# Kernel tuning notes

Hardware: AMD Instinct MI355X
Metric: run time of the kernel (lower is better)

## Reference

```python
import jax, jax.numpy as jnp
import numpy as np
import math

DIM = 2048
N_HEADS = 16
HEAD_DIM = DIM // N_HEADS
BASE = 10000
B, S = 2, 2048


def rope_cache(seq_len, head_dim, base):
    theta = 1.0 / (base ** (jnp.arange(0, head_dim, 2, dtype=jnp.float32)[: head_dim // 2] / head_dim))
    idx_theta = jnp.arange(seq_len, dtype=jnp.float32)[:, None] * theta[None, :]  # [S, D/2]
    return jnp.cos(idx_theta), jnp.sin(idx_theta)


def apply_rope(x, cos, sin):
    # x: [B, S, H, D]; cos/sin: [S, D/2]; interleaved-pair rotation
    b, s, h, d = x.shape
    xr = x.astype(jnp.float32).reshape(b, s, h, d // 2, 2)
    c = cos[None, :, None, :]
    sn = sin[None, :, None, :]
    x0, x1 = xr[..., 0], xr[..., 1]
    out = jnp.stack([x0 * c - x1 * sn, x1 * c + x0 * sn], axis=-1)
    return out.reshape(b, s, h, d).astype(x.dtype)


def setup_inputs() -> dict:
    key = jax.random.key(0)
    k1, k2, k3, k4, k5 = jax.random.split(key, 5)
    x = jax.random.normal(k1, (B, S, DIM), dtype=jnp.float32)
    # causal mask: True = masked out (strict upper triangle)
    mask = jnp.triu(jnp.ones((S, S), dtype=bool), k=1)[None, None]  # [1,1,S,S]
    scale = 0.02
    wq = jax.random.normal(k2, (DIM, DIM), dtype=jnp.float32) * scale
    wk = jax.random.normal(k3, (DIM, DIM), dtype=jnp.float32) * scale
    wv = jax.random.normal(k4, (DIM, DIM), dtype=jnp.float32) * scale
    wo = jax.random.normal(k5, (DIM, DIM), dtype=jnp.float32) * scale
    return {"x": x, "mask": mask, "wq": wq, "wk": wk, "wv": wv, "wo": wo}


def reference(x, mask, wq, wk, wv, wo):
    b, s, _ = x.shape
    cos, sin = rope_cache(s, HEAD_DIM, BASE)
    q = (x @ wq.T).reshape(b, s, N_HEADS, HEAD_DIM)
    k = (x @ wk.T).reshape(b, s, N_HEADS, HEAD_DIM)
    v = (x @ wv.T).reshape(b, s, N_HEADS, HEAD_DIM)
    q = apply_rope(q, cos, sin)
    k = apply_rope(k, cos, sin)
    # [B, H, S, S]
    scores = jnp.einsum('bqhd,bkhd->bhqk', q, k) / math.sqrt(HEAD_DIM)
    scores = jnp.where(mask, -jnp.inf, scores)
    attn = jax.nn.softmax(scores.astype(jnp.float32), axis=-1).astype(q.dtype)
    out = jnp.einsum('bhqk,bkhd->bqhd', attn, v).reshape(b, s, DIM)
    return out @ wo.T
```

## Files before the change

### kernel.cpp

```cpp
#include <hip/hip_runtime.h>
#include <hip/hip_bf16.h>
#include <math.h>

#define DIM   2048
#define NH    16
#define HD    128
#define SEQ   2048
#define BATCH 2
#define QKVN  6144

typedef __attribute__((ext_vector_type(8))) short short8;
typedef __attribute__((ext_vector_type(4))) float f32x4;
typedef __attribute__((ext_vector_type(4))) unsigned int u32x4;
typedef __attribute__((ext_vector_type(4))) _Float16 half4;

static __device__ __forceinline__ unsigned short f2bf(float f) {
    __hip_bfloat16 h = __float2bfloat16(f);
    return *reinterpret_cast<unsigned short*>(&h);
}

static __device__ __forceinline__ void gload16(const void* g, void* l) {
    __builtin_amdgcn_global_load_lds(
        (const __attribute__((address_space(1))) void*)(g),
        (__attribute__((address_space(3))) void*)(l), 16, 0, 0);
}

__device__ __forceinline__ void storeC_helper(float* C, size_t idx, float v) { C[idx] = v; }
__device__ __forceinline__ void storeC_helper(__hip_bfloat16* C, size_t idx, float v) { C[idx] = __float2bfloat16(v); }

__global__ __launch_bounds__(256) void cast_all(const float* __restrict__ x,
                                                const float* __restrict__ wq,
                                                const float* __restrict__ wk,
                                                const float* __restrict__ wv,
                                                const float* __restrict__ wo,
                                                __hip_bfloat16* __restrict__ xb,
                                                __hip_bfloat16* __restrict__ wqkvb,
                                                __hip_bfloat16* __restrict__ wob) {
    const int VX = (BATCH * SEQ * DIM) / 4;
    const int VW = (DIM * DIM) / 4;
    int v = blockIdx.x * blockDim.x + threadIdx.x;
    const float* src; __hip_bfloat16* dst; int off;
    if (v < VX)               { src = x;  dst = xb;                            off = v; }
    else if (v < VX + VW)     { src = wq; dst = wqkvb;                         off = v - VX; }
    else if (v < VX + 2 * VW) { src = wk; dst = wqkvb + (size_t)DIM * DIM;     off = v - VX - VW; }
    else if (v < VX + 3 * VW) { src = wv; dst = wqkvb + 2ull * DIM * DIM;      off = v - VX - 2 * VW; }
    else                      { src = wo; dst = wob;                           off = v - VX - 3 * VW; }
    float4 f = *(const float4*)(src + (size_t)off * 4);
    union { unsigned short u[4]; uint2 d; } pk;
    pk.u[0] = f2bf(f.x); pk.u[1] = f2bf(f.y); pk.u[2] = f2bf(f.z); pk.u[3] = f2bf(f.w);
    *(uint2*)(dst + (size_t)off * 4) = pk.d;
}

template <int MODE, typename OutT>
__global__ __launch_bounds__(256) void gemm_bt(const __hip_bfloat16* __restrict__ A,
                                               const __hip_bfloat16* __restrict__ B,
                                               OutT* __restrict__ C,
                                               _Float16* __restrict__ vt,
                                               int M, int N, int K) {
    constexpr int BK = 64;
    __shared__ __align__(16) __hip_bfloat16 As[128 * BK];
    __shared__ __align__(16) __hip_bfloat16 Bs[128 * BK];
    int tid  = threadIdx.x;
    int lane = tid & 63;
    int wave = tid >> 6;
    int quad = lane >> 4;
    int l15  = lane & 15;
    int wr   = wave >> 1, wc = wave & 1;
    int m0 = blockIdx.y * 128;
    int n0 = blockIdx.x * 128;
    f32x4 acc[4][4] = {};

    for (int k0 = 0; k0 < K; k0 += BK) {
        __syncthreads();
#pragma unroll
        for (int c = 0; c < 4; c++) {
            int br = (wave * 4 + c) * 8;
            int r  = br + (lane >> 3);
            int cc = (lane & 7) ^ (r & 7);
            gload16(A + (size_t)(m0 + r) * K + k0 + cc * 8, As + br * 64);
            gload16(B + (size_t)(n0 + r) * K + k0 + cc * 8, Bs + br * 64);
        }
        __syncthreads();
#pragma unroll
        for (int kk = 0; kk < BK; kk += 32) {
            short8 af[4], bf4[4];
#pragma unroll
            for (int t = 0; t < 4; t++) {
                int Ra = wr * 64 + t * 16 + l15;
                int pa = ((kk >> 3) + quad) ^ (Ra & 7);
                af[t] = *(const short8*)(As + Ra * 64 + pa * 8);
                int Rb = wc * 64 + t * 16 + l15;
                int pb = ((kk >> 3) + quad) ^ (Rb & 7);
                bf4[t] = *(const short8*)(Bs + Rb * 64 + pb * 8);
            }
#pragma unroll
            for (int mt = 0; mt < 4; mt++)
#pragma unroll
                for (int nt = 0; nt < 4; nt++)
                    acc[mt][nt] = __builtin_amdgcn_mfma_f32_16x16x32_bf16(af[mt], bf4[nt], acc[mt][nt], 0, 0, 0);
        }
    }

    if (MODE == 1 && n0 >= 4096) {
        __syncthreads();
        _Float16* T = ((wave < 2) ? (_Float16*)As : (_Float16*)Bs) + (wave & 1) * 4096;
#pragma unroll
        for (int mt = 0; mt < 4; mt++)
#pragma unroll
            for (int nt = 0; nt < 4; nt++) {
                int dcol = nt * 16 + l15;
#pragma unroll
                for (int r = 0; r < 4; r++) {
                    int row = mt * 16 + quad * 4 + r;
                    int chunk = (row >> 3) ^ (dcol & 7);
                    T[dcol * 64 + chunk * 8 + (row & 7)] = (_Float16)acc[mt][nt][r];
                }
            }
        int h = (n0 - 4096) >> 7;
        int b = m0 >> 11;
        int sbase = (m0 & (SEQ - 1)) + wr * 64;
#pragma unroll
        for (int pass = 0; pass < 8; pass++) {
            int dl = pass * 8 + (lane >> 3);
            int sc = lane & 7;
            int chunk = sc ^ (dl & 7);
            u32x4 val = *(const u32x4*)(T + dl * 64 + chunk * 8);
            int d = wc * 64 + dl;
            *(u32x4*)(vt + ((size_t)((b * NH + h) * HD + d)) * SEQ + sbase + sc * 8) = val;
        }
        return;
    }

#pragma unroll
    for (int nt = 0; nt < 4; nt++) {
        int col = n0 + wc * 64 + nt * 16 + l15;
        float theta = 0.f;
        if (MODE == 1)
            theta = __expf(-((float)((col & 127) & ~1) * (1.0f / (float)HD)) * 9.210340371976184f);
#pragma unroll
        for (int mt = 0; mt < 4; mt++)
#pragma unroll
            for (int r = 0; r < 4; r++) {
                int row = m0 + wr * 64 + mt * 16 + quad * 4 + r;
                float val = acc[mt][nt][r];
                if (MODE == 1) {
                    float part = __shfl_xor(val, 1);
                    int s = row & (SEQ - 1);
                    float sn, cs;
                    __sincosf((float)s * theta, &sn, &cs);
                    val = (l15 & 1) ? val * cs + part * sn : val * cs - part * sn;
                }
                storeC_helper(C, (size_t)row * N + col, val);
            }
    }
}

__global__ __launch_bounds__(256, 2) void flash_kernel(const __hip_bfloat16* __restrict__ qkv,
                                                       const _Float16* __restrict__ vt,
                                                       __hip_bfloat16* __restrict__ attn) {
    __shared__ __align__(16) __hip_bfloat16 Ks[2][64 * 128];
    __shared__ __align__(16) _Float16 Vts[2][128 * 64];
    int tid  = threadIdx.x;
    int lane = tid & 63;
    int wl   = tid >> 6;
    int quad = lane >> 4;
    int l15  = lane & 15;
    int qt = 15 - blockIdx.x;
    int bh = blockIdx.y;
    int b  = bh >> 4;
    int h  = bh & 15;
    size_t row0 = (size_t)b * SEQ;
    const _Float16* vbase = vt + (size_t)bh * HD * SEQ;
    const float scale = 0.08838834764831845f;
    const float NEG = -1e30f;

    auto stage = [&](int buf, int kt) {
#pragma unroll
        for (int c = 0; c < 4; c++) {
            int br = (wl * 4 + c) * 4;
            int r  = br + (lane >> 4);
            int cc = (lane & 15) ^ (r & 15);
            gload16(qkv + (row0 + kt * 64 + r) * (size_t)QKVN + DIM + h * HD + cc * 8,
                    &Ks[buf][br * 128]);
        }
#pragma unroll
        for (int c = 0; c < 4; c++) {
            int br = (wl * 4 + c) * 8;
            int r  = br + (lane >> 3);
            int cc = (lane & 7) ^ ((r >> 1) & 7);
            gload16(vbase + (size_t)r * SEQ + kt * 64 + cc * 8, &Vts[buf][br * 64]);
        }
    };

    int ntiles = 2 * (qt + 1);

    short8 qf[2][4];
#pragma unroll
    for (int mt = 0; mt < 2; mt++) {
        int qrow = qt * 128 + wl * 32 + mt * 16 + l15;
        const __hip_bfloat16* qptr = qkv + (row0 + qrow) * (size_t)QKVN + h * HD + quad * 8;
#pragma unroll
        for (int c = 0; c < 4; c++) qf[mt][c] = *(const short8*)(qptr + c * 32);
    }
    f32x4 o[2][8] = {};
    float m_[2] = {NEG, NEG}, l_[2] = {0.f, 0.f};

    stage(0, 0);

    for (int i = 0; i < ntiles; i++) {
        __syncthreads();
        if (i + 1 < ntiles) stage((i + 1) & 1, i + 1);
        const __hip_bfloat16* ks = Ks[i & 1];
        const _Float16* vts = Vts[i & 1];

        f32x4 s[2][4] = {};
#pragma unroll
        for (int ktile = 0; ktile < 4; ktile++) {
            int R = ktile * 16 + l15;
#pragma unroll
            for (int c = 0; c < 4; c++) {
                int phys = (c * 4 + quad) ^ (R & 15);
                short8 kf = *(const short8*)(ks + R * 128 + phys * 8);
                s[0][ktile] = __builtin_amdgcn_mfma_f32_16x16x32_bf16(kf, qf[0][c], s[0][ktile], 0, 0, 0);
                s[1][ktile] = __builtin_amdgcn_mfma_f32_16x16x32_bf16(kf, qf[1][c], s[1][ktile], 0, 0, 0);
            }
        }
        bool diag = (i >= 2 * qt);
        float alpha[2];
#pragma unroll
        for (int mt = 0; mt < 2; mt++) {
            int q = qt * 128 + wl * 32 + mt * 16 + l15;
#pragma unroll
            for (int ktile = 0; ktile < 4; ktile++)
#pragma unroll
                for (int r = 0; r < 4; r++) {
                    float v = s[mt][ktile][r] * scale;
                    if (diag) {
                        int key = i * 64 + ktile * 16 + quad * 4 + r;
                        if (key > q) v = NEG;
                    }
                    s[mt][ktile][r] = v;
                }
            float v = s[mt][0][0];
#pragma unroll
            for (int ktile = 0; ktile < 4; ktile++)
#pragma unroll
                for (int r = 0; r < 4; r++) v = fmaxf(v, s[mt][ktile][r]);
            v = fmaxf(v, __shfl_xor(v, 16));
            v = fmaxf(v, __shfl_xor(v, 32));
            float mnew = fmaxf(m_[mt], v);
            alpha[mt] = __expf(m_[mt] - mnew);
            m_[mt] = mnew;
            float sum = 0.f;
#pragma unroll
            for (int ktile = 0; ktile < 4; ktile++)
#pragma unroll
                for (int r = 0; r < 4; r++) {
                    float p = __expf(s[mt][ktile][r] - mnew);
                    s[mt][ktile][r] = p;
                    sum += p;
                }
            sum += __shfl_xor(sum, 16);
            sum += __shfl_xor(sum, 32);
            l_[mt] = l_[mt] * alpha[mt] + sum;
#pragma unroll
            for (int dt = 0; dt < 8; dt++) o[mt][dt] *= alpha[mt];
        }
        half4 pk[2][4];
#pragma unroll
        for (int mt = 0; mt < 2; mt++)
#pragma unroll
            for (int kc = 0; kc < 4; kc++)
#pragma unroll
                for (int r = 0; r < 4; r++) pk[mt][kc][r] = (_Float16)s[mt][kc][r];
#pragma unroll
        for (int kc = 0; kc < 4; kc++)
#pragma unroll
            for (int dt = 0; dt < 8; dt++) {
                int d = dt * 16 + l15;
                int c4 = ((kc * 4 + quad) ^ (d & 14));
                half4 vf = *(const half4*)(vts + d * 64 + c4 * 4);
                o[0][dt] = __builtin_amdgcn_mfma_f32_16x16x16f16(vf, pk[0][kc], o[0][dt], 0, 0, 0);
                o[1][dt] = __builtin_amdgcn_mfma_f32_16x16x16f16(vf, pk[1][kc], o[1][dt], 0, 0, 0);
            }
    }

    __syncthreads();
    __hip_bfloat16* tw = (__hip_bfloat16*)&Ks[0][0] + wl * 4096;
#pragma unroll
    for (int mt = 0; mt < 2; mt++) {
        float linv = 1.0f / l_[mt];
#pragma unroll
        for (int dt = 0; dt < 8; dt++) {
            int q32 = mt * 16 + l15;
            int c4 = dt * 4 + quad;
            int phys = c4 ^ ((q32 & 7) << 2);
            union { unsigned short u[4]; uint2 dw; } pkb;
#pragma unroll
            for (int r = 0; r < 4; r++) pkb.u[r] = f2bf(o[mt][dt][r] * linv);
            *(uint2*)(tw + q32 * 128 + phys * 4) = pkb.dw;
        }
    }
#pragma unroll
    for (int pass = 0; pass < 8; pass++) {
        int q32 = pass * 4 + (lane >> 4);
        int p = l15;
        int phys = (p * 2) ^ ((q32 & 7) << 2);
        u32x4 val = *(const u32x4*)(tw + q32 * 128 + phys * 4);
        int qg = qt * 128 + wl * 32 + q32;
        *(u32x4*)(attn + (row0 + qg) * (size_t)DIM + h * HD + p * 8) = val;
    }
}

extern "C" void kernel_launch(void* const* d_in, const int* in_sizes, int n_in,
                              void* d_out, int out_size, void* d_ws, size_t ws_size,
                              hipStream_t stream) {
    const float* x  = (const float*)d_in[0];
    const float* wq = (const float*)d_in[2];
    const float* wk = (const float*)d_in[3];
    const float* wv = (const float*)d_in[4];
    const float* wo = (const float*)d_in[5];
    float* out = (float*)d_out;

    char* ws = (char*)d_ws;
    __hip_bfloat16* xb    = (__hip_bfloat16*)(ws);
    __hip_bfloat16* attn  = (__hip_bfloat16*)(ws);
    __hip_bfloat16* wqkvb = (__hip_bfloat16*)(ws + 16777216ull);
    __hip_bfloat16* wob   = (__hip_bfloat16*)(ws + 41943040ull);
    __hip_bfloat16* qkv   = (__hip_bfloat16*)(ws + 50331648ull);
    _Float16*       vtg   = (_Float16*)(ws + 100663296ull);

    const int nv = (BATCH * SEQ * DIM + 4 * DIM * DIM) / 4;
    cast_all<<<nv / 256, 256, 0, stream>>>(x, wq, wk, wv, wo, xb, wqkvb, wob);

    gemm_bt<1, __hip_bfloat16><<<dim3(QKVN / 128, (BATCH * SEQ) / 128), 256, 0, stream>>>(
        xb, wqkvb, qkv, vtg, BATCH * SEQ, QKVN, DIM);

    flash_kernel<<<dim3(16, BATCH * NH), 256, 0, stream>>>(qkv, vtg, attn);

    gemm_bt<0, float><<<dim3(DIM / 128, (BATCH * SEQ) / 128), 256, 0, stream>>>(
        attn, wob, out, nullptr, BATCH * SEQ, DIM, DIM);
}
```

Measured before the change: 417.2 us.

## Balance causal flash attention by pairing light and heavy query tiles per block

Each flash-attention block now handles 64 query rows from two query tiles, qt and 15-qt, processed one after the other. This gives every block the same number of key tiles under the causal mask, instead of some blocks doing far more work than others. Each wave now owns one 16-row MFMA tile instead of two, and the min-blocks-per-CU launch bound is dropped. In exchange, every K/V tile loaded into shared memory serves half as many query rows, so K/V global traffic roughly doubles, and register allocation may shift.

Result: faster. 407.0 us (-2.4%).

```diff
diff --git a/kernel.cpp b/kernel.cpp
--- a/kernel.cpp
+++ b/kernel.cpp
@@ -155,9 +155,9 @@
     }
 }
 
-__global__ __launch_bounds__(256, 2) void flash_kernel(const __hip_bfloat16* __restrict__ qkv,
-                                                       const _Float16* __restrict__ vt,
-                                                       __hip_bfloat16* __restrict__ attn) {
+__global__ __launch_bounds__(256) void flash_kernel(const __hip_bfloat16* __restrict__ qkv,
+                                                    const _Float16* __restrict__ vt,
+                                                    __hip_bfloat16* __restrict__ attn) {
     __shared__ __align__(16) __hip_bfloat16 Ks[2][64 * 128];
     __shared__ __align__(16) _Float16 Vts[2][128 * 64];
     int tid  = threadIdx.x;
@@ -165,7 +165,8 @@
     int wl   = tid >> 6;
     int quad = lane >> 4;
     int l15  = lane & 15;
-    int qt = 15 - blockIdx.x;
+    int pairi = blockIdx.x & 7;
+    int rh    = blockIdx.x >> 3;
     int bh = blockIdx.y;
     int b  = bh >> 4;
     int h  = bh & 15;
@@ -192,123 +193,118 @@
         }
     };
 
-    int ntiles = 2 * (qt + 1);
-
-    short8 qf[2][4];
-#pragma unroll
-    for (int mt = 0; mt < 2; mt++) {
-        int qrow = qt * 128 + wl * 32 + mt * 16 + l15;
-        const __hip_bfloat16* qptr = qkv + (row0 + qrow) * (size_t)QKVN + h * HD + quad * 8;
-#pragma unroll
-        for (int c = 0; c < 4; c++) qf[mt][c] = *(const short8*)(qptr + c * 32);
-    }
-    f32x4 o[2][8] = {};
-    float m_[2] = {NEG, NEG}, l_[2] = {0.f, 0.f};
-
-    stage(0, 0);
-
-    for (int i = 0; i < ntiles; i++) {
-        __syncthreads();
-        if (i + 1 < ntiles) stage((i + 1) & 1, i + 1);
-        const __hip_bfloat16* ks = Ks[i & 1];
-        const _Float16* vts = Vts[i & 1];
-
-        f32x4 s[2][4] = {};
-#pragma unroll
-        for (int ktile = 0; ktile < 4; ktile++) {
-            int R = ktile * 16 + l15;
-#pragma unroll
-            for (int c = 0; c < 4; c++) {
-                int phys = (c * 4 + quad) ^ (R & 15);
-                short8 kf = *(const short8*)(ks + R * 128 + phys * 8);
-                s[0][ktile] = __builtin_amdgcn_mfma_f32_16x16x32_bf16(kf, qf[0][c], s[0][ktile], 0, 0, 0);
-                s[1][ktile] = __builtin_amdgcn_mfma_f32_16x16x32_bf16(kf, qf[1][c], s[1][ktile], 0, 0, 0);
-            }
-        }
-        bool diag = (i >= 2 * qt);
-        float alpha[2];
-#pragma unroll
-        for (int mt = 0; mt < 2; mt++) {
-            int q = qt * 128 + wl * 32 + mt * 16 + l15;
+    for (int seg = 0; seg < 2; seg++) {
+        int qt = seg ? (15 - pairi) : pairi;
+        int ntiles = 2 * (qt + 1);
+
+        short8 qf[4];
+        {
+            int qrow = qt * 128 + rh * 64 + wl * 16 + l15;
+            const __hip_bfloat16* qptr = qkv + (row0 + qrow) * (size_t)QKVN + h * HD + quad * 8;
+#pragma unroll
+            for (int c = 0; c < 4; c++) qf[c] = *(const short8*)(qptr + c * 32);
+        }
+        f32x4 o[8] = {};
+        float m_ = NEG, l_ = 0.f;
+
+        stage(0, 0);
+
+        for (int i = 0; i < ntiles; i++) {
+            __syncthreads();
+            if (i + 1 < ntiles) stage((i + 1) & 1, i + 1);
+            const __hip_bfloat16* ks = Ks[i & 1];
+            const _Float16* vts = Vts[i & 1];
+
+            f32x4 s[4] = {};
+#pragma unroll
+            for (int ktile = 0; ktile < 4; ktile++) {
+                int R = ktile * 16 + l15;
+#pragma unroll
+                for (int c = 0; c < 4; c++) {
+                    int phys = (c * 4 + quad) ^ (R & 15);
+                    short8 kf = *(const short8*)(ks + R * 128 + phys * 8);
+                    s[ktile] = __builtin_amdgcn_mfma_f32_16x16x32_bf16(kf, qf[c], s[ktile], 0, 0, 0);
+                }
+            }
+            bool diag = (i >= 2 * qt);
+            int q = qt * 128 + rh * 64 + wl * 16 + l15;
 #pragma unroll
             for (int ktile = 0; ktile < 4; ktile++)
 #pragma unroll
                 for (int r = 0; r < 4; r++) {
-                    float v = s[mt][ktile][r] * scale;
+                    float v = s[ktile][r] * scale;
                     if (diag) {
                         int key = i * 64 + ktile * 16 + quad * 4 + r;
                         if (key > q) v = NEG;
                     }
-                    s[mt][ktile][r] = v;
-                }
-            float v = s[mt][0][0];
+                    s[ktile][r] = v;
+                }
+            float v = s[0][0];
 #pragma unroll
             for (int ktile = 0; ktile < 4; ktile++)
 #pragma unroll
-                for (int r = 0; r < 4; r++) v = fmaxf(v, s[mt][ktile][r]);
+                for (int r = 0; r < 4; r++) v = fmaxf(v, s[ktile][r]);
             v = fmaxf(v, __shfl_xor(v, 16));
             v = fmaxf(v, __shfl_xor(v, 32));
-            float mnew = fmaxf(m_[mt], v);
-            alpha[mt] = __expf(m_[mt] - mnew);
-            m_[mt] = mnew;
+            float mnew = fmaxf(m_, v);
+            float alpha = __expf(m_ - mnew);
+            m_ = mnew;
             float sum = 0.f;
 #pragma unroll
             for (int ktile = 0; ktile < 4; ktile++)
 #pragma unroll
                 for (int r = 0; r < 4; r++) {
-                    float p = __expf(s[mt][ktile][r] - mnew);
-                    s[mt][ktile][r] = p;
+                    float p = __expf(s[ktile][r] - mnew);
+                    s[ktile][r] = p;
                     sum += p;
                 }
             sum += __shfl_xor(sum, 16);
             sum += __shfl_xor(sum, 32);
-            l_[mt] = l_[mt] * alpha[mt] + sum;
-#pragma unroll
-            for (int dt = 0; dt < 8; dt++) o[mt][dt] *= alpha[mt];
-        }
-        half4 pk[2][4];
-#pragma unroll
-        for (int mt = 0; mt < 2; mt++)
+            l_ = l_ * alpha + sum;
+#pragma unroll
+            for (int dt = 0; dt < 8; dt++) o[dt] *= alpha;
+
+            half4 pk[4];
 #pragma unroll
             for (int kc = 0; kc < 4; kc++)
 #pragma unroll
-                for (int r = 0; r < 4; r++) pk[mt][kc][r] = (_Float16)s[mt][kc][r];
-#pragma unroll
-        for (int kc = 0; kc < 4; kc++)
+                for (int r = 0; r < 4; r++) pk[kc][r] = (_Float16)s[kc][r];
+#pragma unroll
+            for (int kc = 0; kc < 4; kc++)
+#pragma unroll
+                for (int dt = 0; dt < 8; dt++) {
+                    int d = dt * 16 + l15;
+                    int c4 = ((kc * 4 + quad) ^ (d & 14));
+                    half4 vf = *(const half4*)(vts + d * 64 + c4 * 4);
+                    o[dt] = __builtin_amdgcn_mfma_f32_16x16x16f16(vf, pk[kc], o[dt], 0, 0, 0);
+                }
+        }
+
+        __syncthreads();
+        __hip_bfloat16* tw = (__hip_bfloat16*)&Ks[0][0] + wl * 2048;
+        {
+            float linv = 1.0f / l_;
 #pragma unroll
             for (int dt = 0; dt < 8; dt++) {
-                int d = dt * 16 + l15;
-                int c4 = ((kc * 4 + quad) ^ (d & 14));
-                half4 vf = *(const half4*)(vts + d * 64 + c4 * 4);
-                o[0][dt] = __builtin_amdgcn_mfma_f32_16x16x16f16(vf, pk[0][kc], o[0][dt], 0, 0, 0);
-                o[1][dt] = __builtin_amdgcn_mfma_f32_16x16x16f16(vf, pk[1][kc], o[1][dt], 0, 0, 0);
-            }
-    }
-
-    __syncthreads();
-    __hip_bfloat16* tw = (__hip_bfloat16*)&Ks[0][0] + wl * 4096;
-#pragma unroll
-    for (int mt = 0; mt < 2; mt++) {
-        float linv = 1.0f / l_[mt];
-#pragma unroll
-        for (int dt = 0; dt < 8; dt++) {
-            int q32 = mt * 16 + l15;
-            int c4 = dt * 4 + quad;
-            int phys = c4 ^ ((q32 & 7) << 2);
-            union { unsigned short u[4]; uint2 dw; } pkb;
-#pragma unroll
-            for (int r = 0; r < 4; r++) pkb.u[r] = f2bf(o[mt][dt][r] * linv);
-            *(uint2*)(tw + q32 * 128 + phys * 4) = pkb.dw;
-        }
-    }
-#pragma unroll
-    for (int pass = 0; pass < 8; pass++) {
-        int q32 = pass * 4 + (lane >> 4);
-        int p = l15;
-        int phys = (p * 2) ^ ((q32 & 7) << 2);
-        u32x4 val = *(const u32x4*)(tw + q32 * 128 + phys * 4);
-        int qg = qt * 128 + wl * 32 + q32;
-        *(u32x4*)(attn + (row0 + qg) * (size_t)DIM + h * HD + p * 8) = val;
+                int q16 = l15;
+                int c4 = dt * 4 + quad;
+                int phys = c4 ^ ((q16 & 7) << 2);
+                union { unsigned short u[4]; uint2 dw; } pkb;
+#pragma unroll
+                for (int r = 0; r < 4; r++) pkb.u[r] = f2bf(o[dt][r] * linv);
+                *(uint2*)(tw + q16 * 128 + phys * 4) = pkb.dw;
+            }
+        }
+#pragma unroll
+        for (int pass = 0; pass < 4; pass++) {
+            int q16 = pass * 4 + (lane >> 4);
+            int p = l15;
+            int phys = (p * 2) ^ ((q16 & 7) << 2);
+            u32x4 val = *(const u32x4*)(tw + q16 * 128 + phys * 4);
+            int qg = qt * 128 + rh * 64 + wl * 16 + q16;
+            *(u32x4*)(attn + (row0 + qg) * (size_t)DIM + h * HD + p * 8) = val;
+        }
+        __syncthreads();
     }
 }
 
```
